# Kernel optimization log

Measured on AMD Instinct MI355X. Metric: run time of the kernel, lower is better.

Reference implementation:

```python
import jax, jax.numpy as jnp
import numpy as np

D_K = 64
NEG = -1000000000.0

def setup_inputs() -> dict:
    key = jax.random.key(0)
    kq, kk, kv, km = jax.random.split(key, 4)
    B, H, S = 2, 16, 2048
    query = jax.random.normal(kq, (B, H, S, D_K), dtype=jnp.float32)
    k_ = jax.random.normal(kk, (B, H, S, D_K), dtype=jnp.float32)
    value = jax.random.normal(kv, (B, H, S, D_K), dtype=jnp.float32)
    mask = jax.random.randint(km, (1, 1, S, S), 0, 2, dtype=jnp.int32)
    return {"query": query, "key": k_, "value": value, "mask": mask}

def reference(query, key, value, mask):
    # scores: [B,H,S,S]
    scale = jnp.asarray(D_K ** 0.5, dtype=query.dtype)
    scores = jnp.einsum('bhqd,bhkd->bhqk', query, key) / scale
    scores = jnp.where(mask == 0, jnp.asarray(NEG, dtype=scores.dtype), scores)
    proba = jax.nn.softmax(scores, axis=-1)
    return jnp.einsum('bhqk,bhkd->bhqd', proba, value)
```

## Files before the change

### kernel.cpp

```cpp
#include <hip/hip_runtime.h>
#include <hip/hip_bf16.h>
#include <stdint.h>


#define SLEN 2048
#define DK 64
#define KVB 64
#define NT (SLEN / KVB)
#define QTILE 256
#define MFIX 13.0f
#define VPB 136

typedef __attribute__((ext_vector_type(8)))  short    short8;
typedef __attribute__((ext_vector_type(4)))  short    s4v;
typedef __attribute__((ext_vector_type(4)))  unsigned short us4;
typedef __attribute__((ext_vector_type(16))) float    f32x16;
typedef __attribute__((ext_vector_type(4)))  float    float4v;
typedef __attribute__((ext_vector_type(2)))  float    float2v;
typedef __attribute__((ext_vector_type(4)))  unsigned uint4v;
typedef __attribute__((ext_vector_type(4)))  int      int4v;

static __device__ __forceinline__ float fexp2(float x){
#if __has_builtin(__builtin_amdgcn_exp2f)
  return __builtin_amdgcn_exp2f(x);
#else
  float r; asm("v_exp_f32 %0, %1" : "=v"(r) : "v"(x)); return r;
#endif
}
static __device__ __forceinline__ unsigned short f2bfu(float x){
  __hip_bfloat16 h = __float2bfloat16(x);
  return __builtin_bit_cast(unsigned short, h);
}
static __device__ __forceinline__ unsigned pkbf(float lo, float hi){
  return (unsigned)f2bfu(lo) | ((unsigned)f2bfu(hi) << 16);
}
static __device__ __forceinline__ short8 pack8s(float4v a, float4v b, float s){
  short8 r;
  r[0]=(short)f2bfu(a[0]*s); r[1]=(short)f2bfu(a[1]*s);
  r[2]=(short)f2bfu(a[2]*s); r[3]=(short)f2bfu(a[3]*s);
  r[4]=(short)f2bfu(b[0]*s); r[5]=(short)f2bfu(b[1]*s);
  r[6]=(short)f2bfu(b[2]*s); r[7]=(short)f2bfu(b[3]*s);
  return r;
}

__global__ void ScaledDotAttention_mask_pack(const int* __restrict__ mask,
                                             uint32_t* __restrict__ mtw){
  int lane = threadIdx.x & 63;
  int wid  = threadIdx.x >> 6;
  int q    = blockIdx.x * 4 + wid;
  const int* row = mask + (size_t)q * SLEN;
  #pragma unroll 4
  for (int i = 0; i < 32; ++i){
    unsigned long long b = __ballot(row[i*64 + lane] != 0);
    if (lane == 0)
      *(unsigned long long*)(mtw + (size_t)i*4096 + (size_t)q*2) = b;
  }
}

template<bool USE_WS>
__global__ __launch_bounds__(512, 2)
void ScaledDotAttention_attn(const float* __restrict__ Q, const float* __restrict__ K,
                             const float* __restrict__ V, const uint32_t* __restrict__ mtw,
                             const int* __restrict__ mask, float* __restrict__ Out)
{
  __shared__ alignas(16) unsigned short Kl[2][KVB*64];
  __shared__ alignas(16) unsigned short Vt[2][DK*(VPB/2)];

  const int tid  = threadIdx.x;
  const int lane = tid & 63;
  const int l31  = lane & 31;
  const int hi   = lane >> 5;
  const int wid  = __builtin_amdgcn_readfirstlane(tid >> 6);

  const int bid = blockIdx.x;
  const int xcd = bid & 7, ii = bid >> 3;
  const int bh  = xcd + 8*(ii & 3);
  const int qt  = ii >> 2;

  const float* Qb = Q + (size_t)bh*SLEN*DK;
  const float* Kb = K + (size_t)bh*SLEN*DK;
  const float* Vb = V + (size_t)bh*SLEN*DK;

  const int qbase = qt*QTILE + wid*32;
  const float C1 = 0.18033688011112042592f;

  short8 qf[4];
  {
    const float* qrow = Qb + (size_t)(qbase + l31)*DK + hi*8;
    #pragma unroll
    for (int c = 0; c < 4; ++c){
      float4v f0 = *(const float4v*)(qrow + c*16);
      float4v f1 = *(const float4v*)(qrow + c*16 + 4);
      qf[c] = pack8s(f0, f1, C1);
    }
  }

  f32x16 O0, O1;
  #pragma unroll
  for (int r = 0; r < 16; ++r){ O0[r] = 0.f; O1[r] = 0.f; }
  float lsum = 0.f;
  const float vneg = -1.0e9f;

  const int skr  = tid >> 3;
  const int sc8b = tid & 7;
  const int vd   = (tid & 31) * 2;
  const int vk   = (tid >> 5) * 4;
  float4v ka0, ka1;
  float2v vv0, vv1, vv2, vv3;

  auto LOADT = [&](int it){
    const float* kp = Kb + (size_t)it*KVB*DK + skr*DK + sc8b*8;
    ka0 = *(const float4v*)kp;  ka1 = *(const float4v*)(kp + 4);
    const float* vp = Vb + (size_t)it*KVB*DK + vk*DK + vd;
    vv0 = *(const float2v*)vp;
    vv1 = *(const float2v*)(vp + DK);
    vv2 = *(const float2v*)(vp + 2*DK);
    vv3 = *(const float2v*)(vp + 3*DK);
  };

  auto WRITE = [&](int buf){
    short8 kw = pack8s(ka0, ka1, 1.0f);
    int kaddr = (skr*128 + sc8b*16) ^ ((skr & 7) << 4);
    *(short8*)((char*)&Kl[buf][0] + kaddr) = kw;
    us4 r0, r1;
    r0[0]=f2bfu(vv0[0]); r0[1]=f2bfu(vv1[0]); r0[2]=f2bfu(vv2[0]); r0[3]=f2bfu(vv3[0]);
    r1[0]=f2bfu(vv0[1]); r1[1]=f2bfu(vv1[1]); r1[2]=f2bfu(vv2[1]); r1[3]=f2bfu(vv3[1]);
    *(us4*)((char*)&Vt[buf][0] + vd*VPB + vk*2)       = r0;
    *(us4*)((char*)&Vt[buf][0] + (vd+1)*VPB + vk*2)   = r1;
  };

  LOADT(0);
  WRITE(0);
  LOADT(1);
  __syncthreads();
  int cur = 0;

  #pragma unroll 1
  for (int it = 0; it < NT; ++it){
    if (it + 1 < NT) WRITE(cur ^ 1);
    if (it + 2 < NT) LOADT(it + 2);

    uint64_t wv = 0;
    if constexpr (USE_WS){
      wv = *(const uint64_t*)(mtw + (size_t)it*4096 + (size_t)(qbase + l31)*2);
    }

    const unsigned short* Klc = &Kl[cur][0];
    const unsigned short* Vtc = &Vt[cur][0];

    #pragma unroll
    for (int ks = 0; ks < 2; ++ks){
      f32x16 acc;
      #pragma unroll
      for (int r = 0; r < 16; ++r) acc[r] = -MFIX;
      #pragma unroll
      for (int dc = 0; dc < 4; ++dc){
        int kaddr = ((ks*32 + l31)*128 + dc*32 + hi*16) ^ ((l31 & 7) << 4);
        short8 kf = *(const short8*)((const char*)Klc + kaddr);
        acc = __builtin_amdgcn_mfma_f32_32x32x16_bf16(kf, qf[dc], acc, 0, 0, 0);
      }
      float p[16];
      if constexpr (USE_WS){
        uint32_t w = (uint32_t)(wv >> (32*ks)) >> (4*hi);
        #pragma unroll
        for (int r = 0; r < 16; ++r){
          unsigned bit = (w >> ((r & 3) + 8*(r >> 2))) & 1u;
          p[r] = fexp2(bit ? acc[r] : vneg);
        }
      } else {
        const int* mri = mask + (size_t)(qbase + l31)*SLEN + it*KVB + ks*32 + 4*hi;
        int4v g0 = *(const int4v*)(mri);
        int4v g1 = *(const int4v*)(mri + 8);
        int4v g2 = *(const int4v*)(mri + 16);
        int4v g3 = *(const int4v*)(mri + 24);
        #pragma unroll
        for (int r = 0; r < 16; ++r){
          int gi = r >> 2;
          int gv = (gi==0 ? g0[r&3] : gi==1 ? g1[r&3] : gi==2 ? g2[r&3] : g3[r&3]);
          p[r] = fexp2(gv ? acc[r] : vneg);
        }
      }
      float q0 = (p[0]+p[1]) + (p[2]+p[3]);
      float q1 = (p[4]+p[5]) + (p[6]+p[7]);
      float q2 = (p[8]+p[9]) + (p[10]+p[11]);
      float q3 = (p[12]+p[13]) + (p[14]+p[15]);
      lsum += (q0+q1) + (q2+q3);

      #pragma unroll
      for (int kc = 0; kc < 2; ++kc){
        unsigned pw0 = pkbf(p[8*kc+0], p[8*kc+1]);
        unsigned pw1 = pkbf(p[8*kc+2], p[8*kc+3]);
        unsigned pw2 = pkbf(p[8*kc+4], p[8*kc+5]);
        unsigned pw3 = pkbf(p[8*kc+6], p[8*kc+7]);
        uint4v pw; pw[0]=pw0; pw[1]=pw1; pw[2]=pw2; pw[3]=pw3;
        short8 pf = __builtin_bit_cast(short8, pw);
        int kbyte = (ks*32 + kc*16 + 4*hi) * 2;
        #pragma unroll
        for (int hf = 0; hf < 2; ++hf){
          int d = hf*32 + l31;
          int base = d*VPB + kbyte;
          s4v a = *(const s4v*)((const char*)Vtc + base);
          s4v b = *(const s4v*)((const char*)Vtc + base + 16);
          short8 vf;
          #pragma unroll
          for (int j = 0; j < 4; ++j){ vf[j] = a[j]; vf[4+j] = b[j]; }
          if (hf == 0) O0 = __builtin_amdgcn_mfma_f32_32x32x16_bf16(vf, pf, O0, 0, 0, 0);
          else         O1 = __builtin_amdgcn_mfma_f32_32x32x16_bf16(vf, pf, O1, 0, 0, 0);
        }
      }
    }

    __syncthreads();
    cur ^= 1;
  }

  float lt = lsum + __shfl_xor(lsum, 32, 64);
  float rinv = 1.0f / lt;
  float* orow = Out + ((size_t)bh*SLEN + qbase + l31)*DK;
  #pragma unroll
  for (int r = 0; r < 16; ++r){
    int c0 = (r & 3) + 8*(r >> 2) + 4*hi;
    orow[c0]      = O0[r] * rinv;
    orow[c0 + 32] = O1[r] * rinv;
  }
}

extern "C" void kernel_launch(void* const* d_in, const int* in_sizes, int n_in,
                              void* d_out, int out_size, void* d_ws, size_t ws_size,
                              hipStream_t stream) {
  const float* Q    = (const float*)d_in[0];
  const float* K    = (const float*)d_in[1];
  const float* V    = (const float*)d_in[2];
  const int*   mask = (const int*)d_in[3];
  float* Out = (float*)d_out;

  if (ws_size >= (size_t)(SLEN/64) * SLEN * 2 * sizeof(uint32_t)) {
    uint32_t* mtw = (uint32_t*)d_ws;
    ScaledDotAttention_mask_pack<<<dim3(SLEN/4), dim3(256), 0, stream>>>(mask, mtw);
    ScaledDotAttention_attn<true><<<dim3(256), dim3(512), 0, stream>>>(Q, K, V, mtw, mask, Out);
  } else {
    ScaledDotAttention_attn<false><<<dim3(256), dim3(512), 0, stream>>>(Q, K, V, (const uint32_t*)nullptr, mask, Out);
  }
}
```

Baseline: 79.41 us.

## Pre-convert K/V to bf16 LDS images and split KV range across wave groups

Adds a prep kernel that converts K and V once into bf16 tile images (K swizzled, V transposed) in workspace. The main attention kernel then copies those images straight into LDS with global_load_lds, with no per-block fp32 conversion or transpose. It also launches twice as many blocks, each with two wave groups covering half the KV sequence, and merges their partial outputs and row sums through LDS at the end. The aim is to remove redundant per-block conversion work and raise parallelism. The cost is an extra kernel launch, more workspace, and a reduction step, and the new path only runs when the workspace is large enough.

```diff
diff --git a/kernel.cpp b/kernel.cpp
--- a/kernel.cpp
+++ b/kernel.cpp
@@ -6,10 +6,15 @@
 #define SLEN 2048
 #define DK 64
 #define KVB 64
-#define NT (SLEN / KVB)
-#define QTILE 256
+#define NTG 16
 #define MFIX 13.0f
 #define VPB 136
+#define KIMG 8192
+#define VIMG 9216
+#define KOFF (512*1024)
+#define VOFF (KOFF + 32*32*KIMG)
+#define WSNEED ((size_t)VOFF + (size_t)32*32*VIMG)
+#define TILEB (KIMG + VIMG)
 
 typedef __attribute__((ext_vector_type(8)))  short    short8;
 typedef __attribute__((ext_vector_type(4)))  short    s4v;
@@ -41,6 +46,11 @@
   r[4]=(short)f2bfu(b[0]*s); r[5]=(short)f2bfu(b[1]*s);
   r[6]=(short)f2bfu(b[2]*s); r[7]=(short)f2bfu(b[3]*s);
   return r;
+}
+static __device__ __forceinline__ void gload16(const void* g, void* l){
+  __builtin_amdgcn_global_load_lds(
+    (const __attribute__((address_space(1))) void*)g,
+    (__attribute__((address_space(3))) void*)l, 16, 0, 0);
 }
 
 __global__ void ScaledDotAttention_mask_pack(const int* __restrict__ mask,
@@ -57,20 +67,65 @@
   }
 }
 
-template<bool USE_WS>
+__global__ __launch_bounds__(256)
+void ScaledDotAttention_kv_prep(const float* __restrict__ K, const float* __restrict__ V,
+                                uint8_t* __restrict__ ws){
+  __shared__ float vl[64][65];
+  const int bt = blockIdx.x;
+  const int i  = threadIdx.x;
+  const float* Kt = K + ((size_t)(bt >> 5)*SLEN + (bt & 31)*KVB)*DK;
+  const float* Vt = V + ((size_t)(bt >> 5)*SLEN + (bt & 31)*KVB)*DK;
+  uint8_t* Kimg = ws + KOFF + (size_t)bt*KIMG;
+  uint8_t* Vimg = ws + VOFF + (size_t)bt*VIMG;
+  {
+    int d8 = i & 7;
+    #pragma unroll
+    for (int h = 0; h < 2; ++h){
+      int k = (i >> 3) + h*32;
+      const float* src = Kt + k*DK + d8*8;
+      float4v a = *(const float4v*)src, b = *(const float4v*)(src + 4);
+      short8 v = pack8s(a, b, 1.0f);
+      *(short8*)(Kimg + ((k*128 + d8*16) ^ ((k & 7) << 4))) = v;
+    }
+  }
+  {
+    int k = i >> 2, c4 = (i & 3) * 16;
+    const float* src = Vt + k*DK + c4;
+    #pragma unroll
+    for (int c = 0; c < 4; ++c){
+      float4v x = *(const float4v*)(src + c*4);
+      vl[k][c4 + c*4 + 0] = x[0]; vl[k][c4 + c*4 + 1] = x[1];
+      vl[k][c4 + c*4 + 2] = x[2]; vl[k][c4 + c*4 + 3] = x[3];
+    }
+  }
+  __syncthreads();
+  {
+    int d = i >> 2, k0 = (i & 3) * 16;
+    #pragma unroll
+    for (int c = 0; c < 4; ++c){
+      us4 w;
+      w[0] = f2bfu(vl[k0 + c*4 + 0][d]);
+      w[1] = f2bfu(vl[k0 + c*4 + 1][d]);
+      w[2] = f2bfu(vl[k0 + c*4 + 2][d]);
+      w[3] = f2bfu(vl[k0 + c*4 + 3][d]);
+      *(us4*)(Vimg + d*VPB + k0*2 + c*8) = w;
+    }
+  }
+}
+
 __global__ __launch_bounds__(512, 2)
-void ScaledDotAttention_attn(const float* __restrict__ Q, const float* __restrict__ K,
-                             const float* __restrict__ V, const uint32_t* __restrict__ mtw,
-                             const int* __restrict__ mask, float* __restrict__ Out)
-{
-  __shared__ alignas(16) unsigned short Kl[2][KVB*64];
-  __shared__ alignas(16) unsigned short Vt[2][DK*(VPB/2)];
+void ScaledDotAttention_attn_main(const float* __restrict__ Q,
+                                  const uint8_t* __restrict__ ws,
+                                  float* __restrict__ Out){
+  __shared__ alignas(16) char arena[2*2*TILEB];
 
   const int tid  = threadIdx.x;
   const int lane = tid & 63;
   const int l31  = lane & 31;
   const int hi   = lane >> 5;
   const int wid  = __builtin_amdgcn_readfirstlane(tid >> 6);
+  const int g    = wid >> 2;
+  const int wq   = wid & 3;
 
   const int bid = blockIdx.x;
   const int xcd = bid & 7, ii = bid >> 3;
@@ -78,10 +133,7 @@
   const int qt  = ii >> 2;
 
   const float* Qb = Q + (size_t)bh*SLEN*DK;
-  const float* Kb = K + (size_t)bh*SLEN*DK;
-  const float* Vb = V + (size_t)bh*SLEN*DK;
-
-  const int qbase = qt*QTILE + wid*32;
+  const int qbase = qt*128 + wq*32;
   const float C1 = 0.18033688011112042592f;
 
   short8 qf[4];
@@ -101,13 +153,155 @@
   float lsum = 0.f;
   const float vneg = -1.0e9f;
 
+  const uint32_t* mtw = (const uint32_t*)ws;
+
+  auto STAGE = [&](int buf, int it){
+    int kt = g*NTG + it;
+    const uint8_t* Kg = ws + KOFF + (size_t)(bh*32 + kt)*KIMG;
+    const uint8_t* Vg = ws + VOFF + (size_t)(bh*32 + kt)*VIMG;
+    char* Lk = arena + g*(2*TILEB) + buf*TILEB;
+    char* Lv = Lk + KIMG;
+    for (int s = wq; s < 8; s += 4) gload16(Kg + s*1024 + lane*16, Lk + s*1024);
+    for (int s = wq; s < 9; s += 4) gload16(Vg + s*1024 + lane*16, Lv + s*1024);
+  };
+
+  STAGE(0, 0);
+  __syncthreads();
+  int cur = 0;
+
+  #pragma unroll 1
+  for (int it = 0; it < NTG; ++it){
+    if (it + 1 < NTG) STAGE(cur ^ 1, it + 1);
+
+    const int kt = g*NTG + it;
+    uint64_t wv = *(const uint64_t*)(mtw + (size_t)kt*4096 + (size_t)(qbase + l31)*2);
+
+    const char* Klc = arena + g*(2*TILEB) + cur*TILEB;
+    const char* Vtc = Klc + KIMG;
+
+    #pragma unroll
+    for (int ks = 0; ks < 2; ++ks){
+      f32x16 acc;
+      #pragma unroll
+      for (int r = 0; r < 16; ++r) acc[r] = -MFIX;
+      #pragma unroll
+      for (int dc = 0; dc < 4; ++dc){
+        int kaddr = ((ks*32 + l31)*128 + dc*32 + hi*16) ^ ((l31 & 7) << 4);
+        short8 kf = *(const short8*)(Klc + kaddr);
+        acc = __builtin_amdgcn_mfma_f32_32x32x16_bf16(kf, qf[dc], acc, 0, 0, 0);
+      }
+      float p[16];
+      uint32_t w = (uint32_t)(wv >> (32*ks)) >> (4*hi);
+      #pragma unroll
+      for (int r = 0; r < 16; ++r){
+        unsigned bit = (w >> ((r & 3) + 8*(r >> 2))) & 1u;
+        p[r] = fexp2(bit ? acc[r] : vneg);
+      }
+      float q0 = (p[0]+p[1]) + (p[2]+p[3]);
+      float q1 = (p[4]+p[5]) + (p[6]+p[7]);
+      float q2 = (p[8]+p[9]) + (p[10]+p[11]);
+      float q3 = (p[12]+p[13]) + (p[14]+p[15]);
+      lsum += (q0+q1) + (q2+q3);
+
+      #pragma unroll
+      for (int kc = 0; kc < 2; ++kc){
+        unsigned pw0 = pkbf(p[8*kc+0], p[8*kc+1]);
+        unsigned pw1 = pkbf(p[8*kc+2], p[8*kc+3]);
+        unsigned pw2 = pkbf(p[8*kc+4], p[8*kc+5]);
+        unsigned pw3 = pkbf(p[8*kc+6], p[8*kc+7]);
+        uint4v pw; pw[0]=pw0; pw[1]=pw1; pw[2]=pw2; pw[3]=pw3;
+        short8 pf = __builtin_bit_cast(short8, pw);
+        int kbyte = (ks*32 + kc*16 + 4*hi) * 2;
+        #pragma unroll
+        for (int hf = 0; hf < 2; ++hf){
+          int d = hf*32 + l31;
+          int base = d*VPB + kbyte;
+          s4v a = *(const s4v*)(Vtc + base);
+          s4v b = *(const s4v*)(Vtc + base + 16);
+          short8 vf;
+          #pragma unroll
+          for (int j = 0; j < 4; ++j){ vf[j] = a[j]; vf[4+j] = b[j]; }
+          if (hf == 0) O0 = __builtin_amdgcn_mfma_f32_32x32x16_bf16(vf, pf, O0, 0, 0, 0);
+          else         O1 = __builtin_amdgcn_mfma_f32_32x32x16_bf16(vf, pf, O1, 0, 0, 0);
+        }
+      }
+    }
+    __syncthreads();
+    cur ^= 1;
+  }
+
+  lsum = lsum + __shfl_xor(lsum, 32, 64);
+  float* Mg  = (float*)arena;
+  float* smL = (float*)(arena + 128*65*4);
+
+  if (g == 1){
+    float* mg = &Mg[(wq*32 + l31)*65];
+    #pragma unroll
+    for (int r = 0; r < 16; ++r){
+      int c0 = (r & 3) + 8*(r >> 2) + 4*hi;
+      mg[c0]      = O0[r];
+      mg[c0 + 32] = O1[r];
+    }
+    if (hi == 0) smL[wq*32 + l31] = lsum;
+  }
+  __syncthreads();
+  if (g == 0){
+    float lt = lsum + smL[wq*32 + l31];
+    float rinv = 1.0f / lt;
+    const float* mg = &Mg[(wq*32 + l31)*65];
+    float* orow = Out + ((size_t)bh*SLEN + qbase + l31)*DK;
+    #pragma unroll
+    for (int r = 0; r < 16; ++r){
+      int c0 = (r & 3) + 8*(r >> 2) + 4*hi;
+      orow[c0]      = (O0[r] + mg[c0])      * rinv;
+      orow[c0 + 32] = (O1[r] + mg[c0 + 32]) * rinv;
+    }
+  }
+}
+
+template<bool USE_WS>
+__global__ __launch_bounds__(512, 2)
+void ScaledDotAttention_attn_fb(const float* __restrict__ Q, const float* __restrict__ K,
+                                const float* __restrict__ V, const uint32_t* __restrict__ mtw,
+                                const int* __restrict__ mask, float* __restrict__ Out)
+{
+  __shared__ alignas(16) unsigned short Kl[2][KVB*64];
+  __shared__ alignas(16) unsigned short Vt[2][DK*(VPB/2)];
+  const int tid  = threadIdx.x;
+  const int lane = tid & 63;
+  const int l31  = lane & 31;
+  const int hi   = lane >> 5;
+  const int wid  = __builtin_amdgcn_readfirstlane(tid >> 6);
+  const int bid = blockIdx.x;
+  const int xcd = bid & 7, ii = bid >> 3;
+  const int bh  = xcd + 8*(ii & 3);
+  const int qt  = ii >> 2;
+  const float* Qb = Q + (size_t)bh*SLEN*DK;
+  const float* Kb = K + (size_t)bh*SLEN*DK;
+  const float* Vb = V + (size_t)bh*SLEN*DK;
+  const int qbase = qt*256 + wid*32;
+  const float C1 = 0.18033688011112042592f;
+  short8 qf[4];
+  {
+    const float* qrow = Qb + (size_t)(qbase + l31)*DK + hi*8;
+    #pragma unroll
+    for (int c = 0; c < 4; ++c){
+      float4v f0 = *(const float4v*)(qrow + c*16);
+      float4v f1 = *(const float4v*)(qrow + c*16 + 4);
+      qf[c] = pack8s(f0, f1, C1);
+    }
+  }
+  f32x16 O0, O1;
+  #pragma unroll
+  for (int r = 0; r < 16; ++r){ O0[r] = 0.f; O1[r] = 0.f; }
+  float lsum = 0.f;
+  const float vneg = -1.0e9f;
   const int skr  = tid >> 3;
   const int sc8b = tid & 7;
   const int vd   = (tid & 31) * 2;
   const int vk   = (tid >> 5) * 4;
   float4v ka0, ka1;
   float2v vv0, vv1, vv2, vv3;
-
   auto LOADT = [&](int it){
     const float* kp = Kb + (size_t)it*KVB*DK + skr*DK + sc8b*8;
     ka0 = *(const float4v*)kp;  ka1 = *(const float4v*)(kp + 4);
@@ -117,7 +311,6 @@
     vv2 = *(const float2v*)(vp + 2*DK);
     vv3 = *(const float2v*)(vp + 3*DK);
   };
-
   auto WRITE = [&](int buf){
     short8 kw = pack8s(ka0, ka1, 1.0f);
     int kaddr = (skr*128 + sc8b*16) ^ ((skr & 7) << 4);
@@ -125,29 +318,21 @@
     us4 r0, r1;
     r0[0]=f2bfu(vv0[0]); r0[1]=f2bfu(vv1[0]); r0[2]=f2bfu(vv2[0]); r0[3]=f2bfu(vv3[0]);
     r1[0]=f2bfu(vv0[1]); r1[1]=f2bfu(vv1[1]); r1[2]=f2bfu(vv2[1]); r1[3]=f2bfu(vv3[1]);
-    *(us4*)((char*)&Vt[buf][0] + vd*VPB + vk*2)       = r0;
-    *(us4*)((char*)&Vt[buf][0] + (vd+1)*VPB + vk*2)   = r1;
+    *(us4*)((char*)&Vt[buf][0] + vd*VPB + vk*2)     = r0;
+    *(us4*)((char*)&Vt[buf][0] + (vd+1)*VPB + vk*2) = r1;
   };
-
-  LOADT(0);
-  WRITE(0);
-  LOADT(1);
+  LOADT(0); WRITE(0); LOADT(1);
   __syncthreads();
   int cur = 0;
-
   #pragma unroll 1
-  for (int it = 0; it < NT; ++it){
-    if (it + 1 < NT) WRITE(cur ^ 1);
-    if (it + 2 < NT) LOADT(it + 2);
-
+  for (int it = 0; it < 32; ++it){
+    if (it + 1 < 32) WRITE(cur ^ 1);
+    if (it + 2 < 32) LOADT(it + 2);
     uint64_t wv = 0;
-    if constexpr (USE_WS){
+    if constexpr (USE_WS)
       wv = *(const uint64_t*)(mtw + (size_t)it*4096 + (size_t)(qbase + l31)*2);
-    }
-
     const unsigned short* Klc = &Kl[cur][0];
     const unsigned short* Vtc = &Vt[cur][0];
-
     #pragma unroll
     for (int ks = 0; ks < 2; ++ks){
       f32x16 acc;
@@ -185,7 +370,6 @@
       float q2 = (p[8]+p[9]) + (p[10]+p[11]);
       float q3 = (p[12]+p[13]) + (p[14]+p[15]);
       lsum += (q0+q1) + (q2+q3);
-
       #pragma unroll
       for (int kc = 0; kc < 2; ++kc){
         unsigned pw0 = pkbf(p[8*kc+0], p[8*kc+1]);
@@ -209,11 +393,9 @@
         }
       }
     }
-
     __syncthreads();
     cur ^= 1;
   }
-
   float lt = lsum + __shfl_xor(lsum, 32, 64);
   float rinv = 1.0f / lt;
   float* orow = Out + ((size_t)bh*SLEN + qbase + l31)*DK;
@@ -234,11 +416,16 @@
   const int*   mask = (const int*)d_in[3];
   float* Out = (float*)d_out;
 
-  if (ws_size >= (size_t)(SLEN/64) * SLEN * 2 * sizeof(uint32_t)) {
+  if (ws_size >= WSNEED) {
+    uint8_t* ws = (uint8_t*)d_ws;
+    ScaledDotAttention_mask_pack<<<dim3(SLEN/4), dim3(256), 0, stream>>>(mask, (uint32_t*)ws);
+    ScaledDotAttention_kv_prep<<<dim3(1024), dim3(256), 0, stream>>>(K, V, ws);
+    ScaledDotAttention_attn_main<<<dim3(512), dim3(512), 0, stream>>>(Q, ws, Out);
+  } else if (ws_size >= (size_t)(SLEN/64) * SLEN * 2 * sizeof(uint32_t)) {
     uint32_t* mtw = (uint32_t*)d_ws;
     ScaledDotAttention_mask_pack<<<dim3(SLEN/4), dim3(256), 0, stream>>>(mask, mtw);
-    ScaledDotAttention_attn<true><<<dim3(256), dim3(512), 0, stream>>>(Q, K, V, mtw, mask, Out);
+    ScaledDotAttention_attn_fb<true><<<dim3(256), dim3(512), 0, stream>>>(Q, K, V, mtw, mask, Out);
   } else {
-    ScaledDotAttention_attn<false><<<dim3(256), dim3(512), 0, stream>>>(Q, K, V, (const uint32_t*)nullptr, mask, Out);
-  }
-}
+    ScaledDotAttention_attn_fb<false><<<dim3(256), dim3(512), 0, stream>>>(Q, K, V, (const uint32_t*)nullptr, mask, Out);
+  }
+}
```

Result: slower. 96.77 us (+21.8%).
